# Optimization experiments

Hardware: AMD Instinct MI355X
Metric: run time of the kernel (lower is better)

Reference implementation:

```python
import jax, jax.numpy as jnp
import numpy as np

N = 1_000_000   # atoms
E = 4_000_000   # directed edges
G = 1024        # graphs in batch
IN = 64         # input atom feature size
H = 32          # hidden_feats
OUT = 1         # out_feats
EPS = 1e-5


def setup_inputs() -> dict:
    key = jax.random.key(0)
    ks = jax.random.split(key, 16)
    def w(k, shape):
        fan_in = shape[0]
        return jax.random.normal(k, shape, jnp.float32) / np.sqrt(fan_in)
    inp = {}
    inp['feats'] = jax.random.normal(ks[0], (N, IN), jnp.float32)
    inp['src'] = jax.random.randint(ks[1], (E,), 0, N, dtype=jnp.int32)
    inp['dst'] = jax.random.randint(ks[2], (E,), 0, N, dtype=jnp.int32)
    inp['gid'] = jnp.sort(jax.random.randint(ks[3], (N,), 0, G, dtype=jnp.int32))
    # input MLP
    inp['w0'] = w(ks[4], (IN, H)); inp['b0'] = jnp.zeros((H,), jnp.float32)
    inp['g0'] = jnp.ones((H,), jnp.float32); inp['be0'] = jnp.zeros((H,), jnp.float32)
    # block 1: GraphConv + node MLP
    inp['wc1'] = w(ks[5], (H, H)); inp['bc1'] = jnp.zeros((H,), jnp.float32)
    inp['w1'] = w(ks[6], (H, H)); inp['b1'] = jnp.zeros((H,), jnp.float32)
    inp['g1'] = jnp.ones((H,), jnp.float32); inp['be1'] = jnp.zeros((H,), jnp.float32)
    # block 2
    inp['wc2'] = w(ks[7], (H, H)); inp['bc2'] = jnp.zeros((H,), jnp.float32)
    inp['w2'] = w(ks[8], (H, H)); inp['b2'] = jnp.zeros((H,), jnp.float32)
    inp['g2'] = jnp.ones((H,), jnp.float32); inp['be2'] = jnp.zeros((H,), jnp.float32)
    # output head
    inp['wout'] = w(ks[9], (H, OUT)); inp['bout'] = jnp.zeros((OUT,), jnp.float32)
    return inp


def _ln(x, g, b):
    mu = jnp.mean(x, axis=-1, keepdims=True)
    var = jnp.mean(jnp.square(x - mu), axis=-1, keepdims=True)
    return (x - mu) * jax.lax.rsqrt(var + EPS) * g + b


def reference(feats, src, dst, gid,
              w0, b0, g0, be0,
              wc1, bc1, w1, b1, g1, be1,
              wc2, bc2, w2, b2, g2, be2,
              wout, bout):
    elu = jax.nn.elu
    ones_e = jnp.ones((E,), jnp.float32)
    deg_out = jax.ops.segment_sum(ones_e, src, num_segments=N)
    deg_in = jax.ops.segment_sum(ones_e, dst, num_segments=N)
    # dgl norm='both': zero-degree nodes get norm 0
    ns = jnp.where(deg_out > 0, jax.lax.rsqrt(jnp.maximum(deg_out, 1.0)), 0.0)[:, None]
    nd = jnp.where(deg_in > 0, jax.lax.rsqrt(jnp.maximum(deg_in, 1.0)), 0.0)[:, None]

    # input node MLP: Linear -> LayerNorm -> (Dropout p=0) -> ELU
    h = elu(_ln(feats @ w0 + b0, g0, be0))

    for wc, bc, w, b, g, be in ((wc1, bc1, w1, b1, g1, be1),
                                (wc2, bc2, w2, b2, g2, be2)):
        # GraphConv: gather-normalize-scatter then dense transform + ELU
        m = jax.ops.segment_sum((h * ns)[src], dst, num_segments=N) * nd
        h = elu(m @ wc + bc)
        # node MLP block
        h = elu(_ln(h @ w + b, g, be))

    # output head: Linear -> ELU
    h = elu(h @ wout + bout)                 # [N, OUT]
    # dgl.sum_nodes: per-graph readout
    return jax.ops.segment_sum(h, gid, num_segments=G)   # [G, OUT]
```

## Files before the change

kernel.cpp:

```cpp
#include <hip/hip_runtime.h>
#include <math.h>

#define N_ATOMS 1000000
#define N_EDGES 4000000
#define N_GRAPHS 1024
#define IN_F 64
#define HID 32
#define LN_EPS 1e-5f
#define NB 1024
#define PB 512
#define CHUNK ((N_EDGES + PB - 1) / PB)
#define NBUCK_USED 977

typedef unsigned int uint;
typedef unsigned short ushort;

__device__ __forceinline__ float elu_f(float x) {
    return x > 0.0f ? x : expm1f(x);
}
__device__ __forceinline__ uint f2bf(float x) {
    uint u = __float_as_uint(x);
    return (u + 0x7fffu + ((u >> 16) & 1u)) >> 16;
}
__device__ __forceinline__ void acc8(float* a, uint4 u) {
    uint v[4] = {u.x, u.y, u.z, u.w};
#pragma unroll
    for (int r = 0; r < 4; ++r) {
        a[2 * r]     += __uint_as_float(v[r] << 16);
        a[2 * r + 1] += __uint_as_float(v[r] & 0xffff0000u);
    }
}

__global__ __launch_bounds__(256) void hist2(const int* __restrict__ src,
                                             const int* __restrict__ dst,
                                             int* __restrict__ Hs,
                                             int* __restrict__ Hd) {
    __shared__ int hs[NB], hd[NB];
    int blk = blockIdx.x, tid = threadIdx.x;
    for (int i = tid; i < NB; i += 256) { hs[i] = 0; hd[i] = 0; }
    __syncthreads();
    int e0 = blk * CHUNK, e1 = min(N_EDGES, e0 + CHUNK);
    for (int e = e0 + tid; e < e1; e += 256) {
        atomicAdd(&hs[src[e] >> 10], 1);
        atomicAdd(&hd[dst[e] >> 10], 1);
    }
    __syncthreads();
    for (int i = tid; i < NB; i += 256) {
        Hs[blk * NB + i] = hs[i];
        Hd[blk * NB + i] = hd[i];
    }
}

__global__ __launch_bounds__(256) void col_scan(int* __restrict__ H,
                                                int* __restrict__ btot) {
    __shared__ int lds[256];
    int b = blockIdx.x, tid = threadIdx.x;
    int v0 = H[(2 * tid) * NB + b];
    int v1 = H[(2 * tid + 1) * NB + b];
    lds[tid] = v0 + v1;
    __syncthreads();
    for (int off = 1; off < 256; off <<= 1) {
        int t = (tid >= off) ? lds[tid - off] : 0;
        __syncthreads();
        lds[tid] += t;
        __syncthreads();
    }
    int excl = (tid > 0) ? lds[tid - 1] : 0;
    H[(2 * tid) * NB + b] = excl;
    H[(2 * tid + 1) * NB + b] = excl + v0;
    if (tid == 255) btot[b] = excl + v0 + v1;
}

__global__ __launch_bounds__(256) void bucket_scan(const int* __restrict__ btot_d,
                                                   int* __restrict__ bbase_d,
                                                   const int* __restrict__ btot_s,
                                                   int* __restrict__ bbase_s) {
    __shared__ int lds[256];
    const int* in = (blockIdx.x == 0) ? btot_d : btot_s;
    int* out = (blockIdx.x == 0) ? bbase_d : bbase_s;
    int tid = threadIdx.x;
    int v[4]; int s = 0;
#pragma unroll
    for (int q = 0; q < 4; ++q) { v[q] = in[tid * 4 + q]; s += v[q]; }
    lds[tid] = s;
    __syncthreads();
    for (int off = 1; off < 256; off <<= 1) {
        int t = (tid >= off) ? lds[tid - off] : 0;
        __syncthreads();
        lds[tid] += t;
        __syncthreads();
    }
    int run = (tid > 0) ? lds[tid - 1] : 0;
#pragma unroll
    for (int q = 0; q < 4; ++q) { out[tid * 4 + q] = run; run += v[q]; }
    if (tid == 255) out[NB] = run;
}

__global__ __launch_bounds__(256) void scatter_dst(const int* __restrict__ src,
                                                   const int* __restrict__ dst,
                                                   const int* __restrict__ Hd,
                                                   const int* __restrict__ bbase_d,
                                                   int2* __restrict__ pedge) {
    __shared__ int cur[NB];
    int blk = blockIdx.x, tid = threadIdx.x;
    for (int i = tid; i < NB; i += 256) cur[i] = bbase_d[i] + Hd[blk * NB + i];
    __syncthreads();
    int e0 = blk * CHUNK, e1 = min(N_EDGES, e0 + CHUNK);
    for (int e = e0 + tid; e < e1; e += 256) {
        int d = dst[e], s = src[e];
        int pos = atomicAdd(&cur[d >> 10], 1);
        pedge[pos] = make_int2(d, s);
    }
}

__global__ __launch_bounds__(256) void scatter_src(const int* __restrict__ src,
                                                   const int* __restrict__ Hs,
                                                   const int* __restrict__ bbase_s,
                                                   int* __restrict__ psrc) {
    __shared__ int cur[NB];
    int blk = blockIdx.x, tid = threadIdx.x;
    for (int i = tid; i < NB; i += 256) cur[i] = bbase_s[i] + Hs[blk * NB + i];
    __syncthreads();
    int e0 = blk * CHUNK, e1 = min(N_EDGES, e0 + CHUNK);
    for (int e = e0 + tid; e < e1; e += 256) {
        int s = src[e];
        int pos = atomicAdd(&cur[s >> 10], 1);
        psrc[pos] = s;
    }
}

__global__ __launch_bounds__(256) void bucket_csr(const int2* __restrict__ pedge,
                                                  const int* __restrict__ bbase_d,
                                                  int* __restrict__ eidx,
                                                  int* __restrict__ offs) {
    __shared__ int deg[NB];
    __shared__ int cur[NB];
    __shared__ int lds[256];
    int b = blockIdx.x, tid = threadIdx.x;
    int nbase = b << 10;
    if (nbase > N_ATOMS) return;
    int ebase = bbase_d[b], eend = bbase_d[b + 1];
    for (int i = tid; i < NB; i += 256) deg[i] = 0;
    __syncthreads();
    for (int i = ebase + tid; i < eend; i += 256)
        atomicAdd(&deg[pedge[i].x & (NB - 1)], 1);
    __syncthreads();
    int v[4]; int s = 0;
#pragma unroll
    for (int q = 0; q < 4; ++q) { v[q] = deg[tid * 4 + q]; s += v[q]; }
    lds[tid] = s;
    __syncthreads();
    for (int off = 1; off < 256; off <<= 1) {
        int t = (tid >= off) ? lds[tid - off] : 0;
        __syncthreads();
        lds[tid] += t;
        __syncthreads();
    }
    int run = (tid > 0) ? lds[tid - 1] : 0;
#pragma unroll
    for (int q = 0; q < 4; ++q) {
        int l = tid * 4 + q;
        cur[l] = run;
        int node = nbase + l;
        if (node <= N_ATOMS) offs[node] = ebase + run;
        run += v[q];
    }
    __syncthreads();
    for (int i = ebase + tid; i < eend; i += 256) {
        int2 ed = pedge[i];
        int p = atomicAdd(&cur[ed.x & (NB - 1)], 1);
        eidx[ebase + p] = ed.y;
    }
}

__global__ __launch_bounds__(256) void bucket_ns(const int* __restrict__ psrc,
                                                 const int* __restrict__ bbase_s,
                                                 float* __restrict__ ns) {
    __shared__ int deg[NB];
    int b = blockIdx.x, tid = threadIdx.x;
    int nbase = b << 10;
    if (nbase >= N_ATOMS) return;
    int ebase = bbase_s[b], eend = bbase_s[b + 1];
    for (int i = tid; i < NB; i += 256) deg[i] = 0;
    __syncthreads();
    for (int i = ebase + tid; i < eend; i += 256)
        atomicAdd(&deg[psrc[i] & (NB - 1)], 1);
    __syncthreads();
    for (int l = tid; l < NB; l += 256) {
        int node = nbase + l;
        if (node < N_ATOMS) {
            int c = deg[l];
            ns[node] = c > 0 ? rsqrtf((float)c) : 0.0f;
        }
    }
}

__global__ __launch_bounds__(256) void input_mlp(const float* __restrict__ feats,
                                                 const float* __restrict__ w0,
                                                 const float* __restrict__ b0,
                                                 const float* __restrict__ g0,
                                                 const float* __restrict__ be0,
                                                 const float* __restrict__ ns,
                                                 ushort* __restrict__ hs) {
    __shared__ float sw[IN_F * HID];
    int tid = threadIdx.x;
    for (int i = tid; i < IN_F * HID; i += 256) sw[i] = w0[i];
    __syncthreads();

    int node = blockIdx.x * 256 + tid;
    if (node >= N_ATOMS) return;

    const float4* fr = (const float4*)(feats + (size_t)node * IN_F);
    float4 f[16];
#pragma unroll
    for (int q = 0; q < 16; ++q) f[q] = fr[q];

    float acc[HID];
#pragma unroll
    for (int j = 0; j < HID; ++j) acc[j] = b0[j];

#pragma unroll
    for (int q = 0; q < 16; ++q) {
        float vx[4] = {f[q].x, f[q].y, f[q].z, f[q].w};
#pragma unroll
        for (int r = 0; r < 4; ++r) {
            float fv = vx[r];
            const float* wrow = &sw[(q * 4 + r) * HID];
#pragma unroll
            for (int j = 0; j < HID; ++j) acc[j] += fv * wrow[j];
        }
    }

    float mu = 0.0f;
#pragma unroll
    for (int j = 0; j < HID; ++j) mu += acc[j];
    mu *= (1.0f / HID);
    float var = 0.0f;
#pragma unroll
    for (int j = 0; j < HID; ++j) { float d = acc[j] - mu; var += d * d; }
    var *= (1.0f / HID);
    float rs = rsqrtf(var + LN_EPS);

    float os = ns[node];
#pragma unroll
    for (int j = 0; j < HID; ++j)
        acc[j] = elu_f((acc[j] - mu) * rs * g0[j] + be0[j]) * os;

    uint words[HID / 2];
#pragma unroll
    for (int q = 0; q < HID / 2; ++q)
        words[q] = f2bf(acc[2 * q]) | (f2bf(acc[2 * q + 1]) << 16);
    uint4* hv = (uint4*)&hs[(size_t)node * HID];
#pragma unroll
    for (int q = 0; q < 4; ++q)
        hv[q] = make_uint4(words[4 * q], words[4 * q + 1], words[4 * q + 2], words[4 * q + 3]);
}

__global__ __launch_bounds__(256) void spmm4(const ushort* __restrict__ hin,
                                             const int* __restrict__ offs,
                                             const int* __restrict__ eidx,
                                             ushort* __restrict__ m) {
    int t = blockIdx.x * 256 + threadIdx.x;
    int row = t >> 2;
    int l4 = (t & 3) * 8;
    int s0 = offs[row], s1 = offs[row + 1];

    float a[8] = {0.f, 0.f, 0.f, 0.f, 0.f, 0.f, 0.f, 0.f};
    int i = s0;
    for (; i + 8 <= s1; i += 8) {
        int e[8];
#pragma unroll
        for (int q = 0; q < 8; ++q) e[q] = eidx[i + q];
        uint4 r[8];
#pragma unroll
        for (int q = 0; q < 8; ++q) r[q] = *(const uint4*)(hin + (size_t)e[q] * HID + l4);
#pragma unroll
        for (int q = 0; q < 8; ++q) acc8(a, r[q]);
    }
    if (i + 4 <= s1) {
        int e0 = eidx[i], e1 = eidx[i + 1], e2 = eidx[i + 2], e3 = eidx[i + 3];
        uint4 r0 = *(const uint4*)(hin + (size_t)e0 * HID + l4);
        uint4 r1 = *(const uint4*)(hin + (size_t)e1 * HID + l4);
        uint4 r2 = *(const uint4*)(hin + (size_t)e2 * HID + l4);
        uint4 r3 = *(const uint4*)(hin + (size_t)e3 * HID + l4);
        acc8(a, r0); acc8(a, r1); acc8(a, r2); acc8(a, r3);
        i += 4;
    }
    for (; i < s1; ++i) {
        uint4 r0 = *(const uint4*)(hin + (size_t)eidx[i] * HID + l4);
        acc8(a, r0);
    }

    uint w0 = f2bf(a[0]) | (f2bf(a[1]) << 16);
    uint w1 = f2bf(a[2]) | (f2bf(a[3]) << 16);
    uint w2 = f2bf(a[4]) | (f2bf(a[5]) << 16);
    uint w3 = f2bf(a[6]) | (f2bf(a[7]) << 16);
    *(uint4*)(m + (size_t)row * HID + l4) = make_uint4(w0, w1, w2, w3);
}

__global__ __launch_bounds__(256) void mlp_node(const ushort* __restrict__ m,
                                                const int* __restrict__ offs,
                                                const float* __restrict__ wc,
                                                const float* __restrict__ bc,
                                                const float* __restrict__ w,
                                                const float* __restrict__ b,
                                                const float* __restrict__ g,
                                                const float* __restrict__ be,
                                                const float* __restrict__ ns_out,
                                                ushort* __restrict__ hout) {
    __shared__ float swc[HID * HID];
    __shared__ float sww[HID * HID];
    int tid = threadIdx.x;
    for (int i = tid; i < HID * HID; i += 256) { swc[i] = wc[i]; sww[i] = w[i]; }
    __syncthreads();

    int node = blockIdx.x * 256 + tid;
    if (node >= N_ATOMS) return;

    int deg = offs[node + 1] - offs[node];
    float scale = deg > 0 ? rsqrtf((float)deg) : 0.0f;

    const uint4* mr = (const uint4*)(m + (size_t)node * HID);
    uint4 u0 = mr[0], u1 = mr[1], u2 = mr[2], u3 = mr[3];
    float acc[HID];
    {
        uint vv[16] = {u0.x, u0.y, u0.z, u0.w, u1.x, u1.y, u1.z, u1.w,
                       u2.x, u2.y, u2.z, u2.w, u3.x, u3.y, u3.z, u3.w};
#pragma unroll
        for (int r = 0; r < 16; ++r) {
            acc[2 * r]     = __uint_as_float(vv[r] << 16) * scale;
            acc[2 * r + 1] = __uint_as_float(vv[r] & 0xffff0000u) * scale;
        }
    }

    float t1[HID];
#pragma unroll
    for (int j = 0; j < HID; ++j) t1[j] = bc[j];
#pragma unroll 4
    for (int k = 0; k < HID; ++k) {
        float f = acc[k];
#pragma unroll
        for (int j = 0; j < HID; ++j) t1[j] += f * swc[k * HID + j];
    }
#pragma unroll
    for (int j = 0; j < HID; ++j) t1[j] = elu_f(t1[j]);

    float t2[HID];
#pragma unroll
    for (int j = 0; j < HID; ++j) t2[j] = b[j];
#pragma unroll 4
    for (int k = 0; k < HID; ++k) {
        float f = t1[k];
#pragma unroll
        for (int j = 0; j < HID; ++j) t2[j] += f * sww[k * HID + j];
    }

    float mu = 0.0f;
#pragma unroll
    for (int j = 0; j < HID; ++j) mu += t2[j];
    mu *= (1.0f / HID);
    float var = 0.0f;
#pragma unroll
    for (int j = 0; j < HID; ++j) { float d = t2[j] - mu; var += d * d; }
    var *= (1.0f / HID);
    float rs = rsqrtf(var + LN_EPS);

    float os = ns_out ? ns_out[node] : 1.0f;
#pragma unroll
    for (int j = 0; j < HID; ++j)
        t2[j] = elu_f((t2[j] - mu) * rs * g[j] + be[j]) * os;

    uint words[HID / 2];
#pragma unroll
    for (int q = 0; q < HID / 2; ++q)
        words[q] = f2bf(t2[2 * q]) | (f2bf(t2[2 * q + 1]) << 16);
    uint4* hv = (uint4*)&hout[(size_t)node * HID];
#pragma unroll
    for (int q = 0; q < 4; ++q)
        hv[q] = make_uint4(words[4 * q], words[4 * q + 1], words[4 * q + 2], words[4 * q + 3]);
}

__global__ __launch_bounds__(256) void readout(const ushort* __restrict__ h,
                                               const int* __restrict__ gid,
                                               const float* __restrict__ wout,
                                               const float* __restrict__ bout,
                                               float* __restrict__ out) {
    __shared__ float swout[HID];
    __shared__ float buckets[N_GRAPHS];
    __shared__ int s_gf, s_range;
    int base = blockIdx.x * 256;
    int tid = threadIdx.x;
    int nrows = min(256, N_ATOMS - base);

    if (tid < HID) swout[tid] = wout[tid];
    if (tid == 0) {
        int gf = gid[base];
        int gl = gid[base + nrows - 1];
        s_gf = gf;
        s_range = gl - gf + 1;
    }
    __syncthreads();
    int gf = s_gf, range = s_range;
    for (int i = tid; i < range; i += 256) buckets[i] = 0.0f;
    __syncthreads();

    if (tid < nrows) {
        int node = base + tid;
        const uint4* hv = (const uint4*)&h[(size_t)node * HID];
        float acc = bout[0];
#pragma unroll
        for (int q = 0; q < 4; ++q) {
            uint4 u = hv[q];
            uint vv[4] = {u.x, u.y, u.z, u.w};
#pragma unroll
            for (int r = 0; r < 4; ++r) {
                float lo = __uint_as_float(vv[r] << 16);
                float hi = __uint_as_float(vv[r] & 0xffff0000u);
                acc += lo * swout[q * 8 + r * 2] + hi * swout[q * 8 + r * 2 + 1];
            }
        }
        acc = elu_f(acc);
        atomicAdd(&buckets[gid[node] - gf], acc);
    }
    __syncthreads();
    for (int i = tid; i < range; i += 256) {
        float v = buckets[i];
        if (v != 0.0f) atomicAdd(&out[gf + i], v);
    }
}

extern "C" void kernel_launch(void* const* d_in, const int* in_sizes, int n_in,
                              void* d_out, int out_size, void* d_ws, size_t ws_size,
                              hipStream_t stream) {
    const float* feats = (const float*)d_in[0];
    const int* src = (const int*)d_in[1];
    const int* dst = (const int*)d_in[2];
    const int* gid = (const int*)d_in[3];
    const float* w0  = (const float*)d_in[4];
    const float* b0  = (const float*)d_in[5];
    const float* g0  = (const float*)d_in[6];
    const float* be0 = (const float*)d_in[7];
    const float* wc1 = (const float*)d_in[8];
    const float* bc1 = (const float*)d_in[9];
    const float* w1  = (const float*)d_in[10];
    const float* b1  = (const float*)d_in[11];
    const float* g1  = (const float*)d_in[12];
    const float* be1 = (const float*)d_in[13];
    const float* wc2 = (const float*)d_in[14];
    const float* bc2 = (const float*)d_in[15];
    const float* w2  = (const float*)d_in[16];
    const float* b2  = (const float*)d_in[17];
    const float* g2  = (const float*)d_in[18];
    const float* be2 = (const float*)d_in[19];
    const float* wout = (const float*)d_in[20];
    const float* bout = (const float*)d_in[21];
    float* out = (float*)d_out;

    char* ws = (char*)d_ws;
    ushort* X     = (ushort*)(ws + 0);
    ushort* M     = (ushort*)(ws + 64000000);
    int* offs     = (int*)(ws + 128000000);
    int* eidx     = (int*)(ws + 132000064);
    float* ns     = (float*)(ws + 148000064);
    int2* pedge   = (int2*)(ws + 152000064);
    int* psrc     = (int*)(ws + 184000064);
    int* Hd       = (int*)(ws + 200000064);
    int* Hs       = (int*)(ws + 202097216);
    int* btot_d   = (int*)(ws + 204194368);
    int* btot_s   = (int*)(ws + 204198464);
    int* bbase_d  = (int*)(ws + 204202560);
    int* bbase_s  = (int*)(ws + 204207168);

    hipMemsetAsync(out, 0, (size_t)N_GRAPHS * sizeof(float), stream);

    int nb = (N_ATOMS + 255) / 256;
    int sb = (N_ATOMS * 4) / 256;

    hist2<<<PB, 256, 0, stream>>>(src, dst, Hs, Hd);
    col_scan<<<NB, 256, 0, stream>>>(Hd, btot_d);
    col_scan<<<NB, 256, 0, stream>>>(Hs, btot_s);
    bucket_scan<<<2, 256, 0, stream>>>(btot_d, bbase_d, btot_s, bbase_s);
    scatter_dst<<<PB, 256, 0, stream>>>(src, dst, Hd, bbase_d, pedge);
    scatter_src<<<PB, 256, 0, stream>>>(src, Hs, bbase_s, psrc);
    bucket_csr<<<NBUCK_USED, 256, 0, stream>>>(pedge, bbase_d, eidx, offs);
    bucket_ns<<<NBUCK_USED, 256, 0, stream>>>(psrc, bbase_s, ns);

    input_mlp<<<nb, 256, 0, stream>>>(feats, w0, b0, g0, be0, ns, X);

    spmm4<<<sb, 256, 0, stream>>>(X, offs, eidx, M);
    mlp_node<<<nb, 256, 0, stream>>>(M, offs, wc1, bc1, w1, b1, g1, be1, ns, X);
    spmm4<<<sb, 256, 0, stream>>>(X, offs, eidx, M);
    mlp_node<<<nb, 256, 0, stream>>>(M, offs, wc2, bc2, w2, b2, g2, be2, nullptr, X);

    readout<<<nb, 256, 0, stream>>>(X, gid, wout, bout, out);
}
```

Measured before the change: 729.8 us.

## Map input MLP to 32 lanes per node with shuffle-based LayerNorm

Restructures the input MLP so each 32-lane group handles one node, with every lane computing one output feature from a register-resident column of w0. LayerNorm mean and variance are reduced with warp shuffles, and each block loops over 16 nodes per group, so the weight load is spread over more nodes. This drops the per-thread 32-wide accumulator and shared-memory weight staging, which should lower register pressure and LDS traffic. In exchange, every lane reads the full feature row (broadcast loads) and stores are 2-byte scattered writes instead of vectorized 16-byte stores.

```diff
diff --git a/kernel.cpp b/kernel.cpp
--- a/kernel.cpp
+++ b/kernel.cpp
@@ -11,6 +11,7 @@
 #define PB 512
 #define CHUNK ((N_EDGES + PB - 1) / PB)
 #define NBUCK_USED 977
+#define IML_ITER 16
 
 typedef unsigned int uint;
 typedef unsigned short ushort;
@@ -202,58 +203,46 @@
                                                  const float* __restrict__ be0,
                                                  const float* __restrict__ ns,
                                                  ushort* __restrict__ hs) {
-    __shared__ float sw[IN_F * HID];
     int tid = threadIdx.x;
-    for (int i = tid; i < IN_F * HID; i += 256) sw[i] = w0[i];
-    __syncthreads();
-
-    int node = blockIdx.x * 256 + tid;
-    if (node >= N_ATOMS) return;
-
-    const float4* fr = (const float4*)(feats + (size_t)node * IN_F);
-    float4 f[16];
-#pragma unroll
-    for (int q = 0; q < 16; ++q) f[q] = fr[q];
-
-    float acc[HID];
-#pragma unroll
-    for (int j = 0; j < HID; ++j) acc[j] = b0[j];
-
-#pragma unroll
-    for (int q = 0; q < 16; ++q) {
-        float vx[4] = {f[q].x, f[q].y, f[q].z, f[q].w};
-#pragma unroll
-        for (int r = 0; r < 4; ++r) {
-            float fv = vx[r];
-            const float* wrow = &sw[(q * 4 + r) * HID];
-#pragma unroll
-            for (int j = 0; j < HID; ++j) acc[j] += fv * wrow[j];
+    int j = tid & 31;
+    int grp = tid >> 5;
+
+    float wcol[IN_F];
+#pragma unroll
+    for (int k = 0; k < IN_F; ++k) wcol[k] = w0[k * HID + j];
+    float bj = b0[j], gj = g0[j], bej = be0[j];
+
+    int base = blockIdx.x * (8 * IML_ITER) + grp;
+    for (int it = 0; it < IML_ITER; ++it) {
+        int node = base + it * 8;
+        if (node >= N_ATOMS) break;
+
+        const float4* fr = (const float4*)(feats + (size_t)node * IN_F);
+        float a0 = bj, a1 = 0.0f, a2 = 0.0f, a3 = 0.0f;
+#pragma unroll
+        for (int q = 0; q < 16; q += 4) {
+            float4 fA = fr[q], fB = fr[q + 1], fC = fr[q + 2], fD = fr[q + 3];
+            a0 += fA.x * wcol[4*q+0] + fA.y * wcol[4*q+1] + fA.z * wcol[4*q+2] + fA.w * wcol[4*q+3];
+            a1 += fB.x * wcol[4*q+4] + fB.y * wcol[4*q+5] + fB.z * wcol[4*q+6] + fB.w * wcol[4*q+7];
+            a2 += fC.x * wcol[4*q+8] + fC.y * wcol[4*q+9] + fC.z * wcol[4*q+10] + fC.w * wcol[4*q+11];
+            a3 += fD.x * wcol[4*q+12] + fD.y * wcol[4*q+13] + fD.z * wcol[4*q+14] + fD.w * wcol[4*q+15];
         }
-    }
-
-    float mu = 0.0f;
-#pragma unroll
-    for (int j = 0; j < HID; ++j) mu += acc[j];
-    mu *= (1.0f / HID);
-    float var = 0.0f;
-#pragma unroll
-    for (int j = 0; j < HID; ++j) { float d = acc[j] - mu; var += d * d; }
-    var *= (1.0f / HID);
-    float rs = rsqrtf(var + LN_EPS);
-
-    float os = ns[node];
-#pragma unroll
-    for (int j = 0; j < HID; ++j)
-        acc[j] = elu_f((acc[j] - mu) * rs * g0[j] + be0[j]) * os;
-
-    uint words[HID / 2];
-#pragma unroll
-    for (int q = 0; q < HID / 2; ++q)
-        words[q] = f2bf(acc[2 * q]) | (f2bf(acc[2 * q + 1]) << 16);
-    uint4* hv = (uint4*)&hs[(size_t)node * HID];
-#pragma unroll
-    for (int q = 0; q < 4; ++q)
-        hv[q] = make_uint4(words[4 * q], words[4 * q + 1], words[4 * q + 2], words[4 * q + 3]);
+        float acc = (a0 + a1) + (a2 + a3);
+
+        float s = acc;
+        s += __shfl_xor(s, 1); s += __shfl_xor(s, 2); s += __shfl_xor(s, 4);
+        s += __shfl_xor(s, 8); s += __shfl_xor(s, 16);
+        float mu = s * (1.0f / HID);
+        float d = acc - mu;
+        float v = d * d;
+        v += __shfl_xor(v, 1); v += __shfl_xor(v, 2); v += __shfl_xor(v, 4);
+        v += __shfl_xor(v, 8); v += __shfl_xor(v, 16);
+        float rs = rsqrtf(v * (1.0f / HID) + LN_EPS);
+
+        float os = ns[node];
+        float t = elu_f(d * rs * gj + bej) * os;
+        hs[(size_t)node * HID + j] = (ushort)f2bf(t);
+    }
 }
 
 __global__ __launch_bounds__(256) void spmm4(const ushort* __restrict__ hin,
@@ -475,6 +464,7 @@
 
     int nb = (N_ATOMS + 255) / 256;
     int sb = (N_ATOMS * 4) / 256;
+    int ib = (N_ATOMS + 8 * IML_ITER - 1) / (8 * IML_ITER);
 
     hist2<<<PB, 256, 0, stream>>>(src, dst, Hs, Hd);
     col_scan<<<NB, 256, 0, stream>>>(Hd, btot_d);
@@ -485,7 +475,7 @@
     bucket_csr<<<NBUCK_USED, 256, 0, stream>>>(pedge, bbase_d, eidx, offs);
     bucket_ns<<<NBUCK_USED, 256, 0, stream>>>(psrc, bbase_s, ns);
 
-    input_mlp<<<nb, 256, 0, stream>>>(feats, w0, b0, g0, be0, ns, X);
+    input_mlp<<<ib, 256, 0, stream>>>(feats, w0, b0, g0, be0, ns, X);
 
     spmm4<<<sb, 256, 0, stream>>>(X, offs, eidx, M);
     mlp_node<<<nb, 256, 0, stream>>>(M, offs, wc1, bc1, w1, b1, g1, be1, ns, X);
```

Measured after the change: 1.027 ms. 40.7% more time.
